# Kernel tuning notes

Measured on AMD Instinct MI355X. Metric: run time of the kernel, lower is better.

## Reference

```python
import jax, jax.numpy as jnp
import numpy as np

B, S, D = 4, 4096, 1024
H, DK, DV = 8, 128, 128
SEG = 512
DH = 4096
EPS = 1e-5


def setup_inputs() -> dict:
    key = jax.random.key(0)
    ks = jax.random.split(key, 8)
    n = lambda k, shp, sc: (jax.random.normal(k, shp, jnp.float32) * sc)
    return {
        "x": n(ks[0], (B, S, D), 1.0),
        "ln_gamma": jnp.ones((D,), jnp.float32),
        "ln_beta": jnp.zeros((D,), jnp.float32),
        "Wq": n(ks[1], (D, H * DK), 0.02),
        "Wk": n(ks[2], (D, H * DK), 0.02),
        "Wv": n(ks[3], (D, H * DV), 0.02),
        "Wo": n(ks[4], (H * DV, D), 0.02),
        "betas": n(ks[5], (1, H, 1, DV), 1.0),
        "ff_w1": n(ks[6], (D, DH), 0.02),
        "ff_b1": jnp.zeros((DH,), jnp.float32),
        "ff_w2": n(ks[7], (DH, D), 0.02),
        "ff_b2": jnp.zeros((D,), jnp.float32),
    }


def layer_norm(x, gamma, beta):
    mu = x.mean(-1, keepdims=True)
    var = x.var(-1, keepdims=True)
    return (x - mu) * jax.lax.rsqrt(var + EPS) * gamma + beta


def gelu_tanh(x):
    c = np.sqrt(2.0 / np.pi).astype(np.float32)
    return 0.5 * x * (1.0 + jnp.tanh(c * (x + 0.044715 * x * x * x)))


def infini_attention(x, Wq, Wk, Wv, Wo, betas):
    b, s, _ = x.shape
    nseg = s // SEG

    def proj(W, dh):
        # (b,s,H*dh) -> (nseg, b, H, SEG, dh)
        y = (x @ W).reshape(b, nseg, SEG, H, dh)
        return y.transpose(1, 0, 3, 2, 4)

    q = proj(Wq, DK)
    k = proj(Wk, DK)
    v = proj(Wv, DV)

    gate = jax.nn.sigmoid(betas)  # (1,H,1,DV)
    scale = 1.0 / np.sqrt(DK).astype(np.float32)
    causal_mask = jnp.tril(jnp.ones((SEG, SEG), bool))

    def step(carry, qkv):
        mem, z = carry  # (b,H,DK,DV), (b,H,DK,1)
        qs, ks_, vs = qkv  # (b,H,SEG,dk/dv)
        sq = jax.nn.elu(qs) + 1.0
        # compressive-memory retrieval
        att_mem = (sq @ mem) / (sq @ z)  # (b,H,SEG,DV)
        # local (segment) dot-product attention
        scores = jnp.einsum("bhqk,bhsk->bhqs", qs, ks_) * scale
        scores = jnp.where(causal_mask, scores, -jnp.inf)
        att = jax.nn.softmax(scores, axis=-1) @ vs  # (b,H,SEG,DV)
        # linear memory update
        sk = jax.nn.elu(ks_) + 1.0
        mem = mem + jnp.einsum("bhsk,bhsv->bhkv", sk, vs)
        z = z + sk.sum(axis=2)[..., None]
        out = gate * att_mem + (1.0 - gate) * att
        return (mem, z), out

    mem0 = jnp.zeros((b, H, DK, DV), x.dtype)
    z0 = jnp.ones((b, H, DK, 1), x.dtype) / DK
    _, outs = jax.lax.scan(step, (mem0, z0), (q, k, v))
    # (nseg,b,H,SEG,DV) -> (b,s,H*DV)
    outs = outs.transpose(1, 0, 3, 2, 4).reshape(b, s, H * DV)
    return outs @ Wo


def reference(x, ln_gamma, ln_beta, Wq, Wk, Wv, Wo, betas, ff_w1, ff_b1, ff_w2, ff_b2):
    h = layer_norm(x, ln_gamma, ln_beta)
    x = x + infini_attention(h, Wq, Wk, Wv, Wo, betas)
    h = layer_norm(x, ln_gamma, ln_beta)
    ff = gelu_tanh(h @ ff_w1 + ff_b1) @ ff_w2 + ff_b2
    return x + ff
```

## Files before the change

### kernel.cpp

```cpp
#include <hip/hip_runtime.h>

typedef unsigned short u16;
typedef unsigned int   u32;
typedef float f32x4 __attribute__((ext_vector_type(4)));
typedef short bf16x8 __attribute__((ext_vector_type(8)));

#define DEV static __device__ __forceinline__

DEV u16 f2b(float f){
  u32 u = __builtin_bit_cast(u32, f);
  return (u16)((u + 0x7fffu + ((u >> 16) & 1u)) >> 16);
}
DEV float b2f(u16 h){ u32 u = ((u32)h) << 16; return __builtin_bit_cast(float, u); }
DEV u32 pack2(float a, float b){ return (u32)f2b(a) | ((u32)f2b(b) << 16); }
DEV uint4 pack8(const float* f){
  uint4 r; r.x = pack2(f[0],f[1]); r.y = pack2(f[2],f[3]);
  r.z = pack2(f[4],f[5]); r.w = pack2(f[6],f[7]); return r;
}
DEV void unpack8(uint4 u, float* f){
  f[0]=b2f((u16)(u.x&0xffffu)); f[1]=b2f((u16)(u.x>>16));
  f[2]=b2f((u16)(u.y&0xffffu)); f[3]=b2f((u16)(u.y>>16));
  f[4]=b2f((u16)(u.z&0xffffu)); f[5]=b2f((u16)(u.z>>16));
  f[6]=b2f((u16)(u.w&0xffffu)); f[7]=b2f((u16)(u.w>>16));
}
DEV float gelu_t(float x){
  return 0.5f*x*(1.f + tanhf(0.7978845608028654f*(x + 0.044715f*x*x*x)));
}
DEV void g2l16(const u16* g, u16* l){
  __builtin_amdgcn_global_load_lds(
    (const __attribute__((address_space(1))) u32*)g,
    (__attribute__((address_space(3))) u32*)l, 16, 0, 0);
}

__global__ __launch_bounds__(256)
void ln_k(const float* __restrict__ x, const float* __restrict__ gamma,
          const float* __restrict__ beta, u16* __restrict__ out)
{
  const int row = blockIdx.x;
  const int t = threadIdx.x;
  const float4 v = ((const float4*)(x + (size_t)row*1024))[t];
  float s  = v.x+v.y+v.z+v.w;
  float ss = v.x*v.x+v.y*v.y+v.z*v.z+v.w*v.w;
  #pragma unroll
  for (int o=32;o;o>>=1){ s += __shfl_xor(s,o); ss += __shfl_xor(ss,o); }
  __shared__ float rs[4], rq[4];
  if ((t&63)==0){ rs[t>>6]=s; rq[t>>6]=ss; }
  __syncthreads();
  s  = rs[0]+rs[1]+rs[2]+rs[3];
  ss = rq[0]+rq[1]+rq[2]+rq[3];
  const float mean = s*(1.f/1024.f);
  const float var  = ss*(1.f/1024.f) - mean*mean;
  const float inv  = rsqrtf(var + 1e-5f);
  const float4 g4 = ((const float4*)gamma)[t];
  const float4 b4 = ((const float4*)beta)[t];
  float o[4];
  o[0]=(v.x-mean)*inv*g4.x+b4.x; o[1]=(v.y-mean)*inv*g4.y+b4.y;
  o[2]=(v.z-mean)*inv*g4.z+b4.z; o[3]=(v.w-mean)*inv*g4.w+b4.w;
  uint2 w; w.x = pack2(o[0],o[1]); w.y = pack2(o[2],o[3]);
  *(uint2*)(out + (size_t)row*1024 + t*4) = w;
}

__global__ __launch_bounds__(256)
void wconv_k(const float* __restrict__ W, u16* __restrict__ WT, int K, int N)
{
  __shared__ float tile[32][33];
  const int k0 = blockIdx.y<<5, n0 = blockIdx.x<<5;
  const int tx = threadIdx.x & 31, ty = threadIdx.x >> 5;
  #pragma unroll
  for (int r=0;r<32;r+=8)
    tile[ty+r][tx] = W[(size_t)(k0+ty+r)*N + n0+tx];
  __syncthreads();
  #pragma unroll
  for (int r=0;r<32;r+=8)
    WT[(size_t)(n0+ty+r)*K + k0+tx] = f2b(tile[tx][ty+r]);
}

#define EPI_QKV  0
#define EPI_WO   1
#define EPI_GELU 2
#define EPI_FF2  3

template<int EPI>
__global__ __launch_bounds__(512)
void gemm3_k(const u16* __restrict__ A, const u16* __restrict__ BT,
             int K, int lda, int ldb, int N,
             u16* __restrict__ obf, float* __restrict__ of32,
             const float* __restrict__ res, const float* __restrict__ bias)
{
  __shared__ __align__(16) u16 SA[2*4096];
  __shared__ __align__(16) u16 SB[2*8192];
  const int t = threadIdx.x, wid = t>>6, lane = t&63;
  const int c = lane&15, g = lane>>4;
  const int wm = wid>>2, wn = wid&3;
  const int nwg = gridDim.x*gridDim.y;
  const int lb = blockIdx.y*gridDim.x + blockIdx.x;
  const int nl = (lb&7)*(nwg>>3) + (lb>>3);
  const int bx = nl % gridDim.x, by = nl / gridDim.x;
  const int m0 = by<<7, n0 = bx<<8;
  const int srow = lane>>2;
  const int scol = (lane&3)<<3;
  const int sxor = (srow&3)<<3;
  const int rowA = (wid<<4) + srow;
  const u16* aSrc  = A  + (size_t)(m0 + rowA)*lda + (scol ^ sxor);
  const u16* bSrc0 = BT + (size_t)(n0 + rowA)*ldb + (scol ^ sxor);
  const u16* bSrc1 = BT + (size_t)(n0 + 128 + rowA)*ldb + (scol ^ sxor);
  const int kx = (g<<3) ^ ((c&3)<<3);

  f32x4 acc[4][4];
  const f32x4 zz = {0.f,0.f,0.f,0.f};
  #pragma unroll
  for (int i=0;i<4;i++){ acc[i][0]=zz; acc[i][1]=zz; acc[i][2]=zz; acc[i][3]=zz; }

  g2l16(aSrc,  &SA[wid<<9]);
  g2l16(bSrc0, &SB[wid<<9]);
  g2l16(bSrc1, &SB[(wid<<9) + 4096]);
  __syncthreads();

  const int nt = K >> 5;
  for (int tt = 0; tt < nt; ++tt){
    const int cur = tt & 1;
    if (tt + 1 < nt){
      const int ko = (tt+1) << 5;
      g2l16(aSrc + ko,  &SA[((cur^1)<<12) + (wid<<9)]);
      g2l16(bSrc0 + ko, &SB[((cur^1)<<13) + (wid<<9)]);
      g2l16(bSrc1 + ko, &SB[((cur^1)<<13) + (wid<<9) + 4096]);
    }
    bf16x8 af[4], bf[4];
    #pragma unroll
    for (int i=0;i<4;i++)
      af[i] = *(const bf16x8*)&SA[(cur<<12) + ((wm<<6)+(i<<4)+c)*32 + kx];
    #pragma unroll
    for (int j=0;j<4;j++)
      bf[j] = *(const bf16x8*)&SB[(cur<<13) + ((wn<<6)+(j<<4)+c)*32 + kx];
    #pragma unroll
    for (int i=0;i<4;i++)
      #pragma unroll
      for (int j=0;j<4;j++)
        acc[i][j] = __builtin_amdgcn_mfma_f32_16x16x32_bf16(af[i], bf[j], acc[i][j], 0,0,0);
    __syncthreads();
  }

  #pragma unroll
  for (int i=0;i<4;i++){
    const int gr0 = m0 + (wm<<6) + (i<<4) + (g<<2);
    #pragma unroll
    for (int j=0;j<4;j++){
      const int gc = n0 + (wn<<6) + (j<<4) + c;
      #pragma unroll
      for (int r=0;r<4;r++){
        const int gr = gr0 + r;
        const float vv = acc[i][j][r];
        if (EPI==EPI_QKV){
          obf[((size_t)(gc>>10)<<24) + (size_t)gr*1024 + (gc&1023)] = f2b(vv);
        } else if (EPI==EPI_WO){
          const size_t idx = (size_t)gr*N + gc;
          of32[idx] = res[idx] + vv;
        } else if (EPI==EPI_GELU){
          obf[(size_t)gr*N + gc] = f2b(gelu_t(vv + bias[gc]));
        } else {
          const size_t idx = (size_t)gr*N + gc;
          of32[idx] = of32[idx] + vv + (bias ? bias[gc] : 0.f);
        }
      }
    }
  }
}

__global__ __launch_bounds__(256)
void memseg_k(const u16* __restrict__ kb, const u16* __restrict__ vb,
              float* __restrict__ Mseg, float* __restrict__ zseg)
{
  const int bid = blockIdx.x;
  const int seg = bid & 7, h = (bid>>3)&7, b = bid>>6;
  __shared__ __align__(16) u16 Kt[128*64];
  __shared__ __align__(16) u16 Vt[128*64];
  const int t=threadIdx.x, w=t>>6, lane=t&63, c=lane&15, g=lane>>4;

  f32x4 acc[2][8];
  f32x4 zacc[2];
  const f32x4 zzero = {0.f,0.f,0.f,0.f};
  #pragma unroll
  for (int d=0;d<2;d++){ zacc[d]=zzero;
    #pragma unroll
    for (int j=0;j<8;j++) acc[d][j]=zzero; }
  bf16x8 bones;
  { u16 tmp[8];
    #pragma unroll
    for (int e=0;e<8;e++) tmp[e] = (c==0) ? (u16)0x3F80 : (u16)0;
    bones = __builtin_bit_cast(bf16x8, *(uint4*)tmp); }

  for (int s0=0; s0<512; s0+=64){
    __syncthreads();
    {
      const int s = lane, dk0 = w<<5;
      const size_t grow = ((size_t)b*4096 + seg*512 + s0 + s)*1024 + h*128 + dk0;
      #pragma unroll
      for (int jj=0;jj<4;jj++){
        float kf[8], vf[8];
        unpack8(*(const uint4*)(kb + grow + jj*8), kf);
        unpack8(*(const uint4*)(vb + grow + jj*8), vf);
        #pragma unroll
        for (int e=0;e<8;e++){
          const int dk = dk0 + jj*8 + e;
          const float ek = kf[e]>0.f ? kf[e]+1.f : __expf(kf[e]);
          Kt[(dk<<6) + (s ^ ((dk&7)<<3))] = f2b(ek);
          Vt[(dk<<6) + (s ^ ((dk&7)<<3))] = f2b(vf[e]);
        }
      }
    }
    __syncthreads();
    #pragma unroll
    for (int ks=0;ks<2;ks++){
      const int kc = (ks<<5) + (g<<3);
      const bf16x8 a0 = *(const bf16x8*)&Kt[((((w<<1)  )*16 + c)<<6) + (kc ^ ((c&7)<<3))];
      const bf16x8 a1 = *(const bf16x8*)&Kt[((((w<<1)+1)*16 + c)<<6) + (kc ^ ((c&7)<<3))];
      zacc[0] = __builtin_amdgcn_mfma_f32_16x16x32_bf16(a0, bones, zacc[0], 0,0,0);
      zacc[1] = __builtin_amdgcn_mfma_f32_16x16x32_bf16(a1, bones, zacc[1], 0,0,0);
      #pragma unroll
      for (int j=0;j<8;j++){
        const bf16x8 bv = *(const bf16x8*)&Vt[(((j<<4) + c)<<6) + (kc ^ ((c&7)<<3))];
        acc[0][j] = __builtin_amdgcn_mfma_f32_16x16x32_bf16(a0, bv, acc[0][j], 0,0,0);
        acc[1][j] = __builtin_amdgcn_mfma_f32_16x16x32_bf16(a1, bv, acc[1][j], 0,0,0);
      }
    }
  }
  const size_t mb = (size_t)bid*16384;
  #pragma unroll
  for (int d=0;d<2;d++){
    const int dk = ((w<<1)+d)*16 + (g<<2);
    #pragma unroll
    for (int j=0;j<8;j++)
      #pragma unroll
      for (int r=0;r<4;r++)
        Mseg[mb + (size_t)(dk + r)*128 + (j<<4) + c] = acc[d][j][r];
    if (c==0){
      #pragma unroll
      for (int r=0;r<4;r++) zseg[(size_t)bid*128 + dk + r] = zacc[d][r];
    }
  }
}

__global__ __launch_bounds__(256)
void scan_k(const float* __restrict__ Mseg, const float* __restrict__ zseg,
            u16* __restrict__ memBT, float* __restrict__ zB)
{
  const int bh = blockIdx.x >> 3, oct = blockIdx.x & 7;
  const int t = threadIdx.x;
  const int dv = (oct<<4) + (t&15);
  const int kd0 = (t>>4)<<3;
  float run[8];
  #pragma unroll
  for (int i=0;i<8;i++) run[i]=0.f;
  for (int seg=0; seg<8; seg++){
    const size_t base = ((size_t)bh*8 + seg)*16384;
    u16 tmp[8];
    #pragma unroll
    for (int i=0;i<8;i++) tmp[i] = f2b(run[i]);
    *(uint4*)(memBT + base + (size_t)dv*128 + kd0) = *(const uint4*)tmp;
    #pragma unroll
    for (int i=0;i<8;i++) run[i] += Mseg[base + (size_t)(kd0+i)*128 + dv];
  }
  if (oct==0 && t < 128){
    float zr = 1.f/128.f;
    for (int seg=0; seg<8; seg++){
      const size_t base = ((size_t)bh*8 + seg)*128;
      zB[base + t] = zr;
      zr += zseg[base + t];
    }
  }
}

__global__ __launch_bounds__(256,2)
void attn_k(const u16* __restrict__ qb, const u16* __restrict__ kb,
            const u16* __restrict__ vb, const u16* __restrict__ memBT,
            const float* __restrict__ zB, const float* __restrict__ betas,
            u16* __restrict__ attc)
{
  const int bid = blockIdx.x;
  const int s = bid & 255, rt = 7 - (bid >> 8);
  const int seg = s&7, h=(s>>3)&7, b=s>>6;
  __shared__ __align__(16) u16 smem[16384];
  __shared__ __align__(16) u16 Ps[4096];
  u16* Ks = smem;
  u16* Vt = smem + 8192;
  float* zP = (float*)Ps;
  const int t=threadIdx.x, w=t>>6, lane=t&63, c=lane&15, g=lane>>4;
  const size_t base = ((size_t)b*4096 + seg*512)*1024 + h*128;

  bf16x8 af[4];
  {
    const u16* qsrc = qb + base + (size_t)(rt*64 + (w<<4) + c)*1024 + (g<<3);
    #pragma unroll
    for (int ks=0;ks<4;ks++) af[ks] = *(const bf16x8*)(qsrc + ks*32);
  }
  f32x4 acc[8];
  #pragma unroll
  for (int f=0;f<8;f++) acc[f] = (f32x4){0.f,0.f,0.f,0.f};
  float m_run[4], l_run[4];
  #pragma unroll
  for (int r=0;r<4;r++){ m_run[r] = -1e30f; l_run[r] = 0.f; }
  const float scl = 0.08838834764831845f;

  for (int kc=0; kc<=rt; kc++){
    __syncthreads();
    #pragma unroll
    for (int j=0;j<4;j++){
      const int row = (j<<2) + (lane>>4);
      const u16* src = kb + base + (size_t)(kc*64 + (w<<4) + row)*1024
                       + ((size_t)((lane&15) ^ (((w<<4)+row)&7)) << 3);
      g2l16(src, Ks + (((w<<4)+(j<<2))<<7));
    }
    {
      const int kr = lane, d0 = w<<5;
      const u16* vsrc = vb + base + (size_t)(kc*64+kr)*1024 + d0;
      #pragma unroll
      for (int jj=0;jj<4;jj++){
        const uint4 vv = *(const uint4*)(vsrc + jj*8);
        u16 tmp[8]; *(uint4*)tmp = vv;
        #pragma unroll
        for (int e=0;e<8;e++){
          const int dv = d0 + jj*8 + e;
          Vt[(dv<<6) + (kr ^ ((dv&7)<<3))] = tmp[e];
        }
      }
    }
    __syncthreads();
    f32x4 sv[4];
    #pragma unroll
    for (int j=0;j<4;j++) sv[j] = (f32x4){0.f,0.f,0.f,0.f};
    #pragma unroll
    for (int ks=0;ks<4;ks++)
      #pragma unroll
      for (int j=0;j<4;j++){
        const bf16x8 bk = *(const bf16x8*)&Ks[(((j<<4)+c)<<7) + ((((ks<<2)|g) ^ (c&7))<<3)];
        sv[j] = __builtin_amdgcn_mfma_f32_16x16x32_bf16(af[ks], bk, sv[j], 0,0,0);
      }
    const bool diag = (kc==rt);
    float p[4][4], rm[4], rsum[4];
    #pragma unroll
    for (int r=0;r<4;r++){
      float mx = -1e30f;
      #pragma unroll
      for (int j=0;j<4;j++){
        float svv = sv[j][r]*scl;
        if (diag && ((j<<4)+c) > ((w<<4) + (g<<2) + r)) svv = -1e30f;
        p[j][r] = svv;
        mx = fmaxf(mx, svv);
      }
      rm[r] = mx;
    }
    #pragma unroll
    for (int o=1;o<16;o<<=1)
      #pragma unroll
      for (int r=0;r<4;r++) rm[r] = fmaxf(rm[r], __shfl_xor(rm[r], o));
    #pragma unroll
    for (int r=0;r<4;r++){
      const float mn = fmaxf(m_run[r], rm[r]);
      const float sc = __expf(m_run[r] - mn);
      m_run[r] = mn;
      float sum = 0.f;
      #pragma unroll
      for (int j=0;j<4;j++){ p[j][r] = __expf(p[j][r]-mn); sum += p[j][r]; }
      rsum[r] = sum;
      l_run[r] *= sc;
      #pragma unroll
      for (int f=0;f<8;f++) acc[f][r] *= sc;
    }
    #pragma unroll
    for (int o=1;o<16;o<<=1)
      #pragma unroll
      for (int r=0;r<4;r++) rsum[r] += __shfl_xor(rsum[r], o);
    #pragma unroll
    for (int r=0;r<4;r++) l_run[r] += rsum[r];
    #pragma unroll
    for (int j=0;j<4;j++)
      #pragma unroll
      for (int r=0;r<4;r++){
        const int prow = (w<<4)+(g<<2)+r;
        Ps[(prow<<6) + (((j<<4)+c) ^ ((prow&7)<<3))] = f2b(p[j][r]);
      }
    #pragma unroll
    for (int ks2=0; ks2<2; ks2++){
      const bf16x8 pa = *(const bf16x8*)&Ps[(((w<<4)+c)<<6) + ((((ks2<<2)|g) ^ (c&7))<<3)];
      #pragma unroll
      for (int f=0;f<8;f++){
        const int dv = (f<<4)+c;
        const bf16x8 bv = *(const bf16x8*)&Vt[(dv<<6) + ((((ks2<<2)|g) ^ (c&7))<<3)];
        acc[f] = __builtin_amdgcn_mfma_f32_16x16x32_bf16(pa, bv, acc[f], 0,0,0);
      }
    }
  }
  __syncthreads();
  {
    const size_t mbase = (((size_t)b*8+h)*8+seg) << 14;
    #pragma unroll
    for (int i=0;i<8;i++){
      const int row = (i<<2) + (lane>>4);
      const u16* src = memBT + mbase + ((size_t)((w<<5)+row)<<7)
                       + ((size_t)((lane&15) ^ (((w<<5)+row)&7)) << 3);
      g2l16(src, smem + (((w<<5)+(i<<2))<<7));
    }
    if (t < 128) zP[t] = zB[((((size_t)b*8+h)*8+seg)<<7) + t];
  }
  __syncthreads();
  float dpart = 0.f;
  #pragma unroll
  for (int ks=0;ks<4;ks++){
    float f[8]; unpack8(__builtin_bit_cast(uint4, af[ks]), f);
    #pragma unroll
    for (int e=0;e<8;e++){
      f[e] = f[e]>0.f ? f[e]+1.f : __expf(f[e]);
      dpart += f[e] * zP[ks*32 + (g<<3) + e];
    }
    af[ks] = __builtin_bit_cast(bf16x8, pack8(f));
  }
  dpart += __shfl_xor(dpart, 16);
  dpart += __shfl_xor(dpart, 32);
  float den[4];
  #pragma unroll
  for (int r=0;r<4;r++) den[r] = 1.f / __shfl(dpart, (g<<2)+r);
  #pragma unroll 2
  for (int f=0;f<8;f++){
    f32x4 nf = {0.f,0.f,0.f,0.f};
    #pragma unroll
    for (int ks=0;ks<4;ks++){
      const bf16x8 bm = *(const bf16x8*)&smem[(((f<<4)+c)<<7) + ((((ks<<2)|g) ^ (c&7))<<3)];
      nf = __builtin_amdgcn_mfma_f32_16x16x32_bf16(af[ks], bm, nf, 0,0,0);
    }
    const float bv = betas[(h<<7) + (f<<4) + c];
    const float gate = 1.f/(1.f+__expf(-bv));
    #pragma unroll
    for (int r=0;r<4;r++){
      const size_t idx = base + (size_t)(rt*64 + (w<<4) + (g<<2) + r)*1024 + (f<<4) + c;
      const float att = acc[f][r] / l_run[r];
      const float am  = nf[r] * den[r];
      attc[idx] = f2b(gate*am + (1.f-gate)*att);
    }
  }
}

extern "C" void kernel_launch(void* const* d_in, const int* in_sizes, int n_in,
                              void* d_out, int out_size, void* d_ws, size_t ws_size,
                              hipStream_t stream)
{
  (void)in_sizes; (void)n_in; (void)out_size; (void)ws_size;
  const float* x    = (const float*)d_in[0];
  const float* ln_g = (const float*)d_in[1];
  const float* ln_b = (const float*)d_in[2];
  const float* Wq   = (const float*)d_in[3];
  const float* Wk   = (const float*)d_in[4];
  const float* Wv   = (const float*)d_in[5];
  const float* Wo   = (const float*)d_in[6];
  const float* betas= (const float*)d_in[7];
  const float* w1   = (const float*)d_in[8];
  const float* b1   = (const float*)d_in[9];
  const float* w2   = (const float*)d_in[10];
  const float* b2   = (const float*)d_in[11];
  float* out = (float*)d_out;

  char* ws = (char*)d_ws;
  const size_t MB = 1048576;
  u16* qb  = (u16*)(ws);
  u16* kb  = (u16*)(ws + 32*MB);
  u16* vb  = (u16*)(ws + 64*MB);
  u16* Wqkv= (u16*)(ws + 96*MB);
  u16* Wob = (u16*)(ws + 102*MB);
  u16* w1b = (u16*)(ws + 104*MB);
  u16* w2b = (u16*)(ws + 112*MB);
  char* ob = (char*)d_out;
  u16*   h    = (u16*)ob;
  float* Mseg = (float*)(ob + 32*MB);
  u16*   memBT= (u16*)  (ob + 48*MB);
  float* zseg = (float*)(ob + 56*MB);
  float* zB   = (float*)(ob + 56*MB + 131072);
  u16*   at   = qb;
  u16*   h2   = vb;
  u16*   gb2  = qb;

  wconv_k<<<dim3(32,32),256,0,stream>>>(Wq, Wqkv,              1024,1024);
  wconv_k<<<dim3(32,32),256,0,stream>>>(Wk, Wqkv+1024*1024,    1024,1024);
  wconv_k<<<dim3(32,32),256,0,stream>>>(Wv, Wqkv+2*1024*1024,  1024,1024);
  wconv_k<<<dim3(32,32),256,0,stream>>>(Wo, Wob, 1024,1024);
  wconv_k<<<dim3(128,32),256,0,stream>>>(w1, w1b, 1024,4096);
  wconv_k<<<dim3(32,128),256,0,stream>>>(w2, w2b, 4096,1024);

  ln_k<<<16384,256,0,stream>>>(x, ln_g, ln_b, h);
  gemm3_k<EPI_QKV><<<dim3(12,128),512,0,stream>>>(h, Wqkv, 1024,1024,1024, 3072,
                                                  qb, nullptr, nullptr, nullptr);
  memseg_k<<<256,256,0,stream>>>(kb, vb, Mseg, zseg);
  scan_k<<<256,256,0,stream>>>(Mseg, zseg, memBT, zB);
  attn_k<<<2048,256,0,stream>>>(qb, kb, vb, memBT, zB, betas, at);
  gemm3_k<EPI_WO><<<dim3(4,128),512,0,stream>>>(at, Wob, 1024,1024,1024, 1024,
                                                nullptr, out, x, nullptr);
  ln_k<<<16384,256,0,stream>>>(out, ln_g, ln_b, h2);
  for (int cc = 0; cc < 2; cc++){
    gemm3_k<EPI_GELU><<<dim3(8,128),512,0,stream>>>(h2, w1b + (size_t)cc*2048*1024,
                                                    1024,1024,1024, 2048,
                                                    gb2, nullptr, nullptr, b1 + cc*2048);
    gemm3_k<EPI_FF2><<<dim3(4,128),512,0,stream>>>(gb2, w2b + (size_t)cc*2048,
                                                   2048,2048,4096, 1024,
                                                   nullptr, out, nullptr,
                                                   cc==0 ? b2 : nullptr);
  }
}
```

Measured before the change: 709.1 us.

## Enlarge GEMM block tile to 256x256 and use exp-based GELU

The GEMM kernel's M tile grows from 128 to 256 rows. Each warp now computes 128x64 with 8x4 MFMA accumulators, and the A and B shared buffers are both 16 KB per stage. Grids are halved in the M dimension so each block reuses loaded B tiles over twice the rows, which cuts global and LDS traffic per FLOP. The cost is higher register pressure, larger LDS use that may lower occupancy, and fewer blocks for small grids (256 for the 4-wide N launches). Separately, GELU-tanh is rewritten with the identity x*sigmoid(2z) using __expf, which removes the tanhf call.

After: 784.4 us. 1.11x slower.

```diff
diff --git a/kernel.cpp b/kernel.cpp
--- a/kernel.cpp
+++ b/kernel.cpp
@@ -24,7 +24,8 @@
   f[6]=b2f((u16)(u.w&0xffffu)); f[7]=b2f((u16)(u.w>>16));
 }
 DEV float gelu_t(float x){
-  return 0.5f*x*(1.f + tanhf(0.7978845608028654f*(x + 0.044715f*x*x*x)));
+  const float z2 = 1.5957691216057308f*(x + 0.044715f*x*x*x);
+  return x / (1.f + __expf(-z2));
 }
 DEV void g2l16(const u16* g, u16* l){
   __builtin_amdgcn_global_load_lds(
@@ -87,7 +88,7 @@
              u16* __restrict__ obf, float* __restrict__ of32,
              const float* __restrict__ res, const float* __restrict__ bias)
 {
-  __shared__ __align__(16) u16 SA[2*4096];
+  __shared__ __align__(16) u16 SA[2*8192];
   __shared__ __align__(16) u16 SB[2*8192];
   const int t = threadIdx.x, wid = t>>6, lane = t&63;
   const int c = lane&15, g = lane>>4;
@@ -96,24 +97,25 @@
   const int lb = blockIdx.y*gridDim.x + blockIdx.x;
   const int nl = (lb&7)*(nwg>>3) + (lb>>3);
   const int bx = nl % gridDim.x, by = nl / gridDim.x;
-  const int m0 = by<<7, n0 = bx<<8;
+  const int m0 = by<<8, n0 = bx<<8;
   const int srow = lane>>2;
-  const int scol = (lane&3)<<3;
-  const int sxor = (srow&3)<<3;
-  const int rowA = (wid<<4) + srow;
-  const u16* aSrc  = A  + (size_t)(m0 + rowA)*lda + (scol ^ sxor);
-  const u16* bSrc0 = BT + (size_t)(n0 + rowA)*ldb + (scol ^ sxor);
-  const u16* bSrc1 = BT + (size_t)(n0 + 128 + rowA)*ldb + (scol ^ sxor);
+  const int schunk = ((lane&3) ^ (srow&3))<<3;
+  const u16* aSrc0 = A  + (size_t)(m0 + (wid<<5) + srow)*lda + schunk;
+  const u16* bSrc0 = BT + (size_t)(n0 + (wid<<5) + srow)*ldb + schunk;
+  const u16* aSrc1 = aSrc0 + (size_t)16*lda;
+  const u16* bSrc1 = bSrc0 + (size_t)16*ldb;
   const int kx = (g<<3) ^ ((c&3)<<3);
 
-  f32x4 acc[4][4];
-  const f32x4 zz = {0.f,0.f,0.f,0.f};
-  #pragma unroll
-  for (int i=0;i<4;i++){ acc[i][0]=zz; acc[i][1]=zz; acc[i][2]=zz; acc[i][3]=zz; }
-
-  g2l16(aSrc,  &SA[wid<<9]);
-  g2l16(bSrc0, &SB[wid<<9]);
-  g2l16(bSrc1, &SB[(wid<<9) + 4096]);
+  f32x4 acc[8][4];
+  #pragma unroll
+  for (int i=0;i<8;i++)
+    #pragma unroll
+    for (int j=0;j<4;j++) acc[i][j] = (f32x4){0.f,0.f,0.f,0.f};
+
+  g2l16(aSrc0, &SA[(wid<<1)<<9]);
+  g2l16(aSrc1, &SA[((wid<<1)|1)<<9]);
+  g2l16(bSrc0, &SB[(wid<<1)<<9]);
+  g2l16(bSrc1, &SB[((wid<<1)|1)<<9]);
   __syncthreads();
 
   const int nt = K >> 5;
@@ -121,19 +123,21 @@
     const int cur = tt & 1;
     if (tt + 1 < nt){
       const int ko = (tt+1) << 5;
-      g2l16(aSrc + ko,  &SA[((cur^1)<<12) + (wid<<9)]);
-      g2l16(bSrc0 + ko, &SB[((cur^1)<<13) + (wid<<9)]);
-      g2l16(bSrc1 + ko, &SB[((cur^1)<<13) + (wid<<9) + 4096]);
-    }
-    bf16x8 af[4], bf[4];
-    #pragma unroll
-    for (int i=0;i<4;i++)
-      af[i] = *(const bf16x8*)&SA[(cur<<12) + ((wm<<6)+(i<<4)+c)*32 + kx];
+      const int db = (cur^1)<<13;
+      g2l16(aSrc0 + ko, &SA[db + ((wid<<1)<<9)]);
+      g2l16(aSrc1 + ko, &SA[db + (((wid<<1)|1)<<9)]);
+      g2l16(bSrc0 + ko, &SB[db + ((wid<<1)<<9)]);
+      g2l16(bSrc1 + ko, &SB[db + (((wid<<1)|1)<<9)]);
+    }
+    bf16x8 af[8], bf[4];
+    #pragma unroll
+    for (int i=0;i<8;i++)
+      af[i] = *(const bf16x8*)&SA[(cur<<13) + ((wm<<7)+(i<<4)+c)*32 + kx];
     #pragma unroll
     for (int j=0;j<4;j++)
       bf[j] = *(const bf16x8*)&SB[(cur<<13) + ((wn<<6)+(j<<4)+c)*32 + kx];
     #pragma unroll
-    for (int i=0;i<4;i++)
+    for (int i=0;i<8;i++)
       #pragma unroll
       for (int j=0;j<4;j++)
         acc[i][j] = __builtin_amdgcn_mfma_f32_16x16x32_bf16(af[i], bf[j], acc[i][j], 0,0,0);
@@ -141,8 +145,8 @@
   }
 
   #pragma unroll
-  for (int i=0;i<4;i++){
-    const int gr0 = m0 + (wm<<6) + (i<<4) + (g<<2);
+  for (int i=0;i<8;i++){
+    const int gr0 = m0 + (wm<<7) + (i<<4) + (g<<2);
     #pragma unroll
     for (int j=0;j<4;j++){
       const int gc = n0 + (wn<<6) + (j<<4) + c;
@@ -485,21 +489,21 @@
   wconv_k<<<dim3(32,128),256,0,stream>>>(w2, w2b, 4096,1024);
 
   ln_k<<<16384,256,0,stream>>>(x, ln_g, ln_b, h);
-  gemm3_k<EPI_QKV><<<dim3(12,128),512,0,stream>>>(h, Wqkv, 1024,1024,1024, 3072,
-                                                  qb, nullptr, nullptr, nullptr);
+  gemm3_k<EPI_QKV><<<dim3(12,64),512,0,stream>>>(h, Wqkv, 1024,1024,1024, 3072,
+                                                 qb, nullptr, nullptr, nullptr);
   memseg_k<<<256,256,0,stream>>>(kb, vb, Mseg, zseg);
   scan_k<<<256,256,0,stream>>>(Mseg, zseg, memBT, zB);
   attn_k<<<2048,256,0,stream>>>(qb, kb, vb, memBT, zB, betas, at);
-  gemm3_k<EPI_WO><<<dim3(4,128),512,0,stream>>>(at, Wob, 1024,1024,1024, 1024,
-                                                nullptr, out, x, nullptr);
+  gemm3_k<EPI_WO><<<dim3(4,64),512,0,stream>>>(at, Wob, 1024,1024,1024, 1024,
+                                               nullptr, out, x, nullptr);
   ln_k<<<16384,256,0,stream>>>(out, ln_g, ln_b, h2);
   for (int cc = 0; cc < 2; cc++){
-    gemm3_k<EPI_GELU><<<dim3(8,128),512,0,stream>>>(h2, w1b + (size_t)cc*2048*1024,
-                                                    1024,1024,1024, 2048,
-                                                    gb2, nullptr, nullptr, b1 + cc*2048);
-    gemm3_k<EPI_FF2><<<dim3(4,128),512,0,stream>>>(gb2, w2b + (size_t)cc*2048,
-                                                   2048,2048,4096, 1024,
-                                                   nullptr, out, nullptr,
-                                                   cc==0 ? b2 : nullptr);
-  }
-}
+    gemm3_k<EPI_GELU><<<dim3(8,64),512,0,stream>>>(h2, w1b + (size_t)cc*2048*1024,
+                                                   1024,1024,1024, 2048,
+                                                   gb2, nullptr, nullptr, b1 + cc*2048);
+    gemm3_k<EPI_FF2><<<dim3(4,64),512,0,stream>>>(gb2, w2b + (size_t)cc*2048,
+                                                  2048,2048,4096, 1024,
+                                                  nullptr, out, nullptr,
+                                                  cc==0 ? b2 : nullptr);
+  }
+}
```
